# Performance work log

Measured on AMD Instinct MI355X. Metric: run time of the kernel, lower is better.

## Reference

```python
import jax, jax.numpy as jnp
import numpy as np

B = 512
M = 50
N = 50
G = 1            # args.g
ITER = 4         # args.iter_50
EPS = 1e-8


def image2matrix_vit(x):
    # x: [b,1,28,28] -> [b,49,16] (4x4 non-overlapping patches, row-major)
    b = x.shape[0]
    t = x[:, 0].reshape(b, 7, 4, 7, 4)
    return t.transpose(0, 1, 3, 2, 4).reshape(b, 49, 16)


def maxpool2d(x, kh, kw, sh, sw):
    # x: [b,1,H,W], VALID max pooling (matches F.max_pool2d)
    return jax.lax.reduce_window(x, -jnp.inf, jax.lax.max,
                                 (1, 1, kh, kw), (1, 1, sh, sw), 'VALID')


def optical_mvm(inp, w, full_sig):
    # inp: [b,50,50] normalized input, w: [b,50,50] normalized weight (pre-transpose)
    w = jnp.swapaxes(w, 1, 2)
    indim1 = inp.shape[1]       # 50
    odim2 = w.shape[1]          # 50
    out_row = inp.shape[-2]     # 50
    A = jnp.repeat(jnp.repeat(inp, G, axis=1), ITER, axis=2)   # [b,50,200]
    Bm = jnp.repeat(jnp.repeat(w, G, axis=1), ITER, axis=2)    # [b,50,200]
    pr = (4 * M - A.shape[-2]) // 2
    pc = (4 * N - A.shape[-1]) // 2
    A = jnp.pad(A, ((0, 0), (pr, pr), (pc, pc)))               # [b,200,200]
    Bm = jnp.pad(Bm, ((0, 0), (pr, pr), (pc, pc)))
    # precomputed reference spectrum (args.fft_sig_50)
    fft_sig = jnp.fft.fftshift(jnp.fft.fft(full_sig, axis=0), axes=0)
    fft_full = jnp.fft.fftshift(jnp.fft.fft(full_sig[None] * A, axis=1), axes=1)
    opc = fft_full * Bm
    opc_fft = jnp.abs(jnp.fft.fftshift(jnp.fft.fft(opc, axis=2), axes=2))
    r0, r1 = 2 * M - odim2, 2 * M + odim2          # 50:150
    c0, c1 = 2 * N + N // indim1, 3 * N + 3        # 101:153
    temp = opc_fft[:, r0:r1, c0:c1][:, None]       # [b,1,100,52]
    Cmat = maxpool2d(temp, 2, 3, 2, N // indim1)   # [b,1,50,50]
    amp = jnp.abs(fft_sig)[r0:r1, c0:c1][None, None]
    amp = maxpool2d(amp, 2, 3, 2, N // indim1)     # [1,1,50,50]
    amp = amp / (jnp.max(amp) + EPS)
    res = jnp.abs(Cmat / amp)[:, 0]                # [b,50,50]
    res = res / (jnp.max(res, axis=(1, 2), keepdims=True) + EPS)
    return jnp.swapaxes(res, 1, 2)[:, :out_row, :odim2]


def matrix_multiply_optical(inp, w, full_sig):
    # inp: [b,50,50]; w: [50,50] (already abs+padded)
    b = inp.shape[0]
    wb = jnp.broadcast_to(w.T[None], (b,) + w.T.shape)       # [b,50,50]
    imax = jnp.max(inp, axis=-1, keepdims=True)              # [b,50,1]
    inpn = inp / (imax + EPS)
    wmax = jnp.max(wb, axis=-2, keepdims=True)               # [b,1,50]
    wn = wb / (wmax + EPS)
    max_multi = imax @ wmax                                  # [b,50,50]
    out = optical_mvm(inpn, wn, full_sig).astype(jnp.float32)
    return out * max_multi


def setup_inputs() -> dict:
    key = jax.random.key(0)
    k1, k2, k3, k4 = jax.random.split(key, 4)
    inp = jax.random.uniform(k1, (B, 1, 28, 28), dtype=jnp.float32)
    weight = jax.random.normal(k2, (50, 16), dtype=jnp.float32) * 0.1
    bias = jax.random.normal(k3, (1, 49, 50), dtype=jnp.float32) * 0.01
    full_sig = jax.random.uniform(k4, (4 * M, 4 * N), dtype=jnp.float32)
    return {"input": inp, "weight": weight, "bias": bias, "full_sig": full_sig}


def reference(input, weight, bias, full_sig):
    x = image2matrix_vit(input)                  # [b,49,16]
    w = jnp.abs(weight)                          # exp_type != 'standard_mmm'
    out1 = x.shape[1]                            # 49
    x = jnp.pad(x, ((0, 0), (0, 50 - x.shape[1]), (0, 50 - x.shape[2])))
    w = jnp.pad(w, ((0, 50 - w.shape[0]), (0, 50 - w.shape[1])))
    out = matrix_multiply_optical(x, w, full_sig)
    return out[:, :out1, :50] + bias             # bias broadcasts over batch
```

## Files before the change

### kernel.cpp

```cpp
#include <hip/hip_runtime.h>
#include <math.h>

#define EPS 1e-8f
#define TWOPI 6.2831853071795864769f

typedef _Float16 h8 __attribute__((ext_vector_type(8)));
typedef float f32x16 __attribute__((ext_vector_type(16)));

#define WS_WMAX 0
#define WS_WN   64
#define WS_RCPA 1024
#define WS_A2   8192
#define WS_B3   16384


__global__ __launch_bounds__(256) void k_prelude(const float* __restrict__ w,
                                                 const float* __restrict__ fs,
                                                 float* __restrict__ ws) {
    const int blk = blockIdx.x, t = threadIdx.x;
    if (blk < 163) {
        __shared__ float tc[200], tsn[200];
        for (int i = t; i < 200; i += 256) {
            float s, c;
            sincosf(-TWOPI * (float)i / 200.f, &s, &c);
            tc[i] = c; tsn[i] = s;
        }
        __syncthreads();
        int gid = blk * 256 + t;
        int q = gid >> 3, part = gid & 7;
        float aR = 0.f, aI = 0.f;
        if (q < 5200) {
            int s_ = q / 52, u = q - s_ * 52;
            int k = (150 + s_) % 200;
            int j = 101 + u;
            int ph = (k * (part * 25)) % 200;
            for (int r = part * 25; r < part * 25 + 25; ++r) {
                float v = fs[r * 200 + j];
                aR = fmaf(v, tc[ph], aR);
                aI = fmaf(v, tsn[ph], aI);
                ph += k; if (ph >= 200) ph -= 200;
            }
        }
        aR += __shfl_xor(aR, 1); aI += __shfl_xor(aI, 1);
        aR += __shfl_xor(aR, 2); aI += __shfl_xor(aI, 2);
        aR += __shfl_xor(aR, 4); aI += __shfl_xor(aI, 4);
        if (q < 5200 && part == 0)
            ws[WS_RCPA + q] = 1.0f / sqrtf(aR * aR + aI * aI);
    } else {
        int gid = (blk - 163) * 256 + t;
        if (gid < 50) {
            float mx = 0.f, vals[16];
            for (int q = 0; q < 16; ++q) {
                float v = fabsf(w[gid * 16 + q]);
                vals[q] = v; mx = fmaxf(mx, v);
            }
            ws[WS_WMAX + gid] = mx;
            float d = mx + EPS;
            for (int q = 0; q < 16; ++q) ws[WS_WN + gid * 16 + q] = vals[q] / d;
        }
        _Float16* A2h = (_Float16*)(ws + WS_A2);
        for (int a = gid; a < 16384; a += 4096) {
            int s = a & 7, l = (a >> 3) & 63, pks = (a >> 9) & 7, tm = a >> 12;
            int part = pks >> 2;
            int row = 32 * tm + (l & 31);
            int k = 16 * (pks & 3) + 8 * (l >> 5) + s;
            float X = 0.f;
            if (row < 100 && k < 49) {
                int m = (row < 50) ? row : row - 50;
                int kk = (175 + m) % 200;
                int ph = (kk * (75 + k)) % 200;
                float sn, cs;
                sincosf(-TWOPI * (float)ph / 200.f, &sn, &cs);
                X = (row < 50) ? cs : sn;
            }
            _Float16 hi = (_Float16)X;
            A2h[a] = part ? (_Float16)(X - (float)hi) : hi;
        }
        _Float16* B3h = (_Float16*)(ws + WS_B3);
        for (int bI = gid; bI < 32768; bI += 4096) {
            int s = bI & 7, l = (bI >> 3) & 63, pks = (bI >> 9) & 15, tn = bI >> 13;
            int part = pks >> 3;
            int np = 32 * tn + (l & 31);
            int kap = 16 * (pks & 7) + 8 * (l >> 5) + s;
            float X = 0.f;
            if (np < 104) {
                int cc = np >> 1;
                int j = kap & 63;
                int ph = ((cc + 1) * j) % 200;
                float sn, cs;
                sincosf(-TWOPI * (float)ph / 200.f, &sn, &cs);
                X = (np & 1) ? ((kap < 64) ? sn : cs) : ((kap < 64) ? cs : -sn);
            }
            _Float16 hi = (_Float16)X;
            B3h[bI] = part ? (_Float16)(X - (float)hi) : hi;
        }
    }
}

__global__ __launch_bounds__(512, 4) void k_main(const float* __restrict__ in,
                                                 const float* __restrict__ bias,
                                                 const float* __restrict__ fs,
                                                 const float* __restrict__ ws,
                                                 float* __restrict__ out) {
    __shared__ __align__(16) char R1[16384];
    __shared__ __align__(16) char R2[32768];
    __shared__ float xpat[50][16];
    __shared__ float imax_s[50];
    __shared__ float inv_s[50];
    __shared__ float res_s[26][50];
    __shared__ __align__(16) float red8[8];

    const int t = threadIdx.x;
    const int b = blockIdx.x;
    const int lane = t & 63;
    const int wid = t >> 6;
    const int swid = __builtin_amdgcn_readfirstlane(wid);
    const float* ib = in + b * 784;

    if (t < 196) {
        int row = t >> 2, s4 = t & 3;
        int pr = row / 7, pc = row - pr * 7;
        float4 v4 = *(const float4*)(ib + (pr * 4 + s4) * 28 + pc * 4);
        *(float4*)(&xpat[row][s4 * 4]) = v4;
        float mx = fmaxf(fmaxf(v4.x, v4.y), fmaxf(v4.z, v4.w));
        mx = fmaxf(mx, __shfl_xor(mx, 1));
        mx = fmaxf(mx, __shfl_xor(mx, 2));
        if (s4 == 0) { imax_s[row] = mx; inv_s[row] = 1.f / (mx + EPS); }
    }
    __syncthreads();

    {
        const int l = t & 63;
        const int ksq = (t >> 6) & 3;
        const int tn = t >> 8;
        const int j = (l & 31) + 32 * tn;
        const int i0 = 16 * ksq + 8 * (l >> 5);
        h8 hiv, lov;
        #pragma unroll
        for (int s = 0; s < 8; ++s) {
            int i = i0 + s;
            float v = 0.f;
            if (i < 49) v = fs[(75 + i) * 200 + j] * xpat[i][j >> 2] * inv_s[i];
            _Float16 hi = (_Float16)v;
            hiv[s] = hi;
            lov[s] = (_Float16)(v - (float)hi);
        }
        _Float16* B2h = (_Float16*)R1;
        const int base0 = ((tn * 8 + ksq) * 64 + l) * 8;
        *(h8*)(B2h + base0) = hiv;
        *(h8*)(B2h + base0 + 2048) = lov;
    }
    __syncthreads();

    {
        const int tm = swid >> 1, tn = swid & 1;
        f32x16 acc;
        #pragma unroll
        for (int i = 0; i < 16; ++i) acc[i] = 0.f;
        const h8* wsA2 = (const h8*)(ws + WS_A2);
        #pragma unroll
        for (int ks = 0; ks < 12; ++ks) {
            int pA = (ks < 4) ? ks : ks - 4;
            int pB = (ks < 8) ? ks : ks - 8;
            h8 a = wsA2[(tm * 8 + pA) * 64 + lane];
            h8 bf = *(const h8*)(R1 + (((tn * 8 + pB) * 64 + lane) << 4));
            acc = __builtin_amdgcn_mfma_f32_32x32x16_f16(a, bf, acc, 0, 0, 0);
        }
        const float* wn = ws + WS_WN;
        const int j = (lane & 31) + 32 * tn;
        const int q = j >> 2;
        _Float16* A3h = (_Float16*)R2;
        #pragma unroll
        for (int r = 0; r < 16; ++r) {
            int row = (r & 3) + 8 * (r >> 2) + 4 * (lane >> 5) + 32 * tm;
            if (row < 100) {
                int m = (row < 50) ? row : row - 50;
                float v = acc[r] * wn[m * 16 + q];
                _Float16 hi = (_Float16)v;
                int kap = j + ((row < 50) ? 0 : 64);
                int tm3 = m >> 5;
                int pks = kap >> 4;
                int lslot = (m & 31) + 32 * ((kap >> 3) & 1);
                int base = ((tm3 * 16 + pks) * 64 + lslot) * 8 + (kap & 7);
                A3h[base] = hi;
                A3h[base + 4096] = (_Float16)(v - (float)hi);
            }
        }
    }
    __syncthreads();

    {
        const int tm3 = swid >> 2, tn3 = swid & 3;
        f32x16 acc;
        #pragma unroll
        for (int i = 0; i < 16; ++i) acc[i] = 0.f;
        const h8* wsB3 = (const h8*)(ws + WS_B3);
        #pragma unroll
        for (int ks = 0; ks < 24; ++ks) {
            int pA = (ks < 8) ? ks : ks - 8;
            int pB = (ks < 16) ? ks : ks - 16;
            h8 a = *(const h8*)(R2 + (((tm3 * 16 + pA) * 64 + lane) << 4));
            h8 bf = wsB3[(tn3 * 16 + pB) * 64 + lane];
            acc = __builtin_amdgcn_mfma_f32_32x32x16_f16(a, bf, acc, 0, 0, 0);
        }
        const int np = (lane & 31) + 32 * tn3;
        float* aG = (float*)R1;
        if (np < 104) {
            const int cc = np >> 1;
            const bool wr = !(np & 1);
            #pragma unroll
            for (int r = 0; r < 16; ++r) {
                int row = (r & 3) + 8 * (r >> 2) + 4 * (lane >> 5) + 32 * tm3;
                float g = acc[r];
                float gp = __shfl_xor(g, 1);
                if (row < 50 && wr) aG[row * 52 + cc] = sqrtf(g * g + gp * gp);
            }
        }
    }
    __syncthreads();

    const float* ra = ws + WS_RCPA;
    const float* aG = (const float*)R1;
    float local = 0.f;
    for (int o = t; o < 1300; o += 512) {
        int hh = o / 50, w2 = o - hh * 50;
        int h = hh + 12;
        int m1 = 2 * h - 25, m2 = m1 + 1;
        float v = 0.f;
        #pragma unroll
        for (int du = 0; du < 3; ++du) {
            int u = w2 + du;
            if (m1 >= 0) v = fmaxf(v, aG[m1 * 52 + u]);
            if (m2 < 50) v = fmaxf(v, aG[m2 * 52 + u]);
        }
        float rc = ra[(2 * h) * 52 + w2];
        #pragma unroll
        for (int du = 1; du < 3; ++du) rc = fminf(rc, ra[(2 * h) * 52 + w2 + du]);
        #pragma unroll
        for (int du = 0; du < 3; ++du) rc = fminf(rc, ra[(2 * h + 1) * 52 + w2 + du]);
        float r = v * rc;
        res_s[hh][w2] = r;
        local = fmaxf(local, r);
    }
    #pragma unroll
    for (int off = 32; off > 0; off >>= 1)
        local = fmaxf(local, __shfl_xor(local, off));
    if (lane == 0) red8[wid] = local;
    __syncthreads();

    float mres;
    {
        float4 r0 = *(const float4*)&red8[0];
        float4 r1 = *(const float4*)&red8[4];
        float m0 = fmaxf(fmaxf(r0.x, r0.y), fmaxf(r0.z, r0.w));
        float m1 = fmaxf(fmaxf(r1.x, r1.y), fmaxf(r1.z, r1.w));
        mres = fmaxf(m0, m1);
    }
    float invm = 1.f / (mres + EPS);

    const float* wmaxg = ws + WS_WMAX;
    for (int o = t; o < 2450; o += 512) {
        int r = o / 50, c = o - r * 50;
        float val = bias[o];
        if (c >= 12 && c < 38)
            val = fmaf(res_s[c - 12][r] * invm, imax_s[r] * wmaxg[c], val);
        out[b * 2450 + o] = val;
    }
}

extern "C" void kernel_launch(void* const* d_in, const int* in_sizes, int n_in,
                              void* d_out, int out_size, void* d_ws, size_t ws_size,
                              hipStream_t stream) {
    const float* in   = (const float*)d_in[0];
    const float* w    = (const float*)d_in[1];
    const float* bias = (const float*)d_in[2];
    const float* fs   = (const float*)d_in[3];
    float* out = (float*)d_out;
    float* ws  = (float*)d_ws;

    hipLaunchKernelGGL(k_prelude, dim3(179),  dim3(256), 0, stream, w, fs, ws);
    hipLaunchKernelGGL(k_main,    dim3(512),  dim3(512), 0, stream, in, bias, fs, ws, out);
}
```

Measured before the change: 25.99 us.

## Drop split-fp16 on one operand of each GEMM and pad LDS layout

Both MFMA GEMM stages previously used hi+lo fp16 splitting on both operands (three MFMA products per step). Now one operand per GEMM is stored as plain fp16 and only the other keeps its hi/lo split, which cuts the MFMA count from 12 to 8 and from 24 to 16. The work is spread over two independent accumulators. The A3 LDS tile shrinks to half size with a padded stride of 65 to avoid bank conflicts, and it is zero-initialized up front. The prelude grid grows so each thread writes a single A2 element. The trade-off is reduced precision on the DFT-twiddle or intermediate operand.

```diff
diff --git a/kernel.cpp b/kernel.cpp
--- a/kernel.cpp
+++ b/kernel.cpp
@@ -58,12 +58,12 @@
             float d = mx + EPS;
             for (int q = 0; q < 16; ++q) ws[WS_WN + gid * 16 + q] = vals[q] / d;
         }
-        _Float16* A2h = (_Float16*)(ws + WS_A2);
-        for (int a = gid; a < 16384; a += 4096) {
-            int s = a & 7, l = (a >> 3) & 63, pks = (a >> 9) & 7, tm = a >> 12;
-            int part = pks >> 2;
+        {
+            _Float16* A2h = (_Float16*)(ws + WS_A2);
+            int a = gid;
+            int s = a & 7, l = (a >> 3) & 63, pks = (a >> 9) & 3, tm = a >> 11;
             int row = 32 * tm + (l & 31);
-            int k = 16 * (pks & 3) + 8 * (l >> 5) + s;
+            int k = 16 * pks + 8 * (l >> 5) + s;
             float X = 0.f;
             if (row < 100 && k < 49) {
                 int m = (row < 50) ? row : row - 50;
@@ -73,11 +73,10 @@
                 sincosf(-TWOPI * (float)ph / 200.f, &sn, &cs);
                 X = (row < 50) ? cs : sn;
             }
-            _Float16 hi = (_Float16)X;
-            A2h[a] = part ? (_Float16)(X - (float)hi) : hi;
+            A2h[a] = (_Float16)X;
         }
         _Float16* B3h = (_Float16*)(ws + WS_B3);
-        for (int bI = gid; bI < 32768; bI += 4096) {
+        for (int bI = gid; bI < 32768; bI += 8192) {
             int s = bI & 7, l = (bI >> 3) & 63, pks = (bI >> 9) & 15, tn = bI >> 13;
             int part = pks >> 3;
             int np = 32 * tn + (l & 31);
@@ -103,7 +102,7 @@
                                                  const float* __restrict__ ws,
                                                  float* __restrict__ out) {
     __shared__ __align__(16) char R1[16384];
-    __shared__ __align__(16) char R2[32768];
+    __shared__ __align__(16) char R2[16640];
     __shared__ float xpat[50][16];
     __shared__ float imax_s[50];
     __shared__ float inv_s[50];
@@ -127,6 +126,12 @@
         mx = fmaxf(mx, __shfl_xor(mx, 2));
         if (s4 == 0) { imax_s[row] = mx; inv_s[row] = 1.f / (mx + EPS); }
     }
+    {
+        h8 z;
+        #pragma unroll
+        for (int s = 0; s < 8; ++s) z[s] = (_Float16)0.f;
+        for (int o = t; o < 1040; o += 512) *(h8*)(R2 + (o << 4)) = z;
+    }
     __syncthreads();
 
     {
@@ -154,18 +159,19 @@
 
     {
         const int tm = swid >> 1, tn = swid & 1;
-        f32x16 acc;
-        #pragma unroll
-        for (int i = 0; i < 16; ++i) acc[i] = 0.f;
+        f32x16 acc0, acc1;
+        #pragma unroll
+        for (int i = 0; i < 16; ++i) { acc0[i] = 0.f; acc1[i] = 0.f; }
         const h8* wsA2 = (const h8*)(ws + WS_A2);
         #pragma unroll
-        for (int ks = 0; ks < 12; ++ks) {
-            int pA = (ks < 4) ? ks : ks - 4;
-            int pB = (ks < 8) ? ks : ks - 8;
-            h8 a = wsA2[(tm * 8 + pA) * 64 + lane];
-            h8 bf = *(const h8*)(R1 + (((tn * 8 + pB) * 64 + lane) << 4));
-            acc = __builtin_amdgcn_mfma_f32_32x32x16_f16(a, bf, acc, 0, 0, 0);
-        }
+        for (int kq = 0; kq < 4; ++kq) {
+            h8 a   = wsA2[(tm * 4 + kq) * 64 + lane];
+            h8 bhi = *(const h8*)(R1 + (((tn * 8 + kq) * 64 + lane) << 4));
+            h8 blo = *(const h8*)(R1 + (((tn * 8 + kq + 4) * 64 + lane) << 4));
+            acc0 = __builtin_amdgcn_mfma_f32_32x32x16_f16(a, bhi, acc0, 0, 0, 0);
+            acc1 = __builtin_amdgcn_mfma_f32_32x32x16_f16(a, blo, acc1, 0, 0, 0);
+        }
+        f32x16 acc = acc0 + acc1;
         const float* wn = ws + WS_WN;
         const int j = (lane & 31) + 32 * tn;
         const int q = j >> 2;
@@ -176,14 +182,12 @@
             if (row < 100) {
                 int m = (row < 50) ? row : row - 50;
                 float v = acc[r] * wn[m * 16 + q];
-                _Float16 hi = (_Float16)v;
                 int kap = j + ((row < 50) ? 0 : 64);
                 int tm3 = m >> 5;
                 int pks = kap >> 4;
-                int lslot = (m & 31) + 32 * ((kap >> 3) & 1);
-                int base = ((tm3 * 16 + pks) * 64 + lslot) * 8 + (kap & 7);
-                A3h[base] = hi;
-                A3h[base + 4096] = (_Float16)(v - (float)hi);
+                int bb = (kap >> 3) & 1;
+                int elem = ((tm3 * 8 + pks) * 65 + (m & 31) + 33 * bb) * 8 + (kap & 7);
+                A3h[elem] = (_Float16)v;
             }
         }
     }
@@ -191,18 +195,20 @@
 
     {
         const int tm3 = swid >> 2, tn3 = swid & 3;
-        f32x16 acc;
-        #pragma unroll
-        for (int i = 0; i < 16; ++i) acc[i] = 0.f;
+        f32x16 acc0, acc1;
+        #pragma unroll
+        for (int i = 0; i < 16; ++i) { acc0[i] = 0.f; acc1[i] = 0.f; }
         const h8* wsB3 = (const h8*)(ws + WS_B3);
-        #pragma unroll
-        for (int ks = 0; ks < 24; ++ks) {
-            int pA = (ks < 8) ? ks : ks - 8;
-            int pB = (ks < 16) ? ks : ks - 16;
-            h8 a = *(const h8*)(R2 + (((tm3 * 16 + pA) * 64 + lane) << 4));
-            h8 bf = wsB3[(tn3 * 16 + pB) * 64 + lane];
-            acc = __builtin_amdgcn_mfma_f32_32x32x16_f16(a, bf, acc, 0, 0, 0);
-        }
+        const int aoff = lane + (lane >> 5);
+        #pragma unroll
+        for (int kq = 0; kq < 8; ++kq) {
+            h8 a   = *(const h8*)(R2 + (((tm3 * 8 + kq) * 65 + aoff) << 4));
+            h8 bhi = wsB3[(tn3 * 16 + kq) * 64 + lane];
+            h8 blo = wsB3[(tn3 * 16 + kq + 8) * 64 + lane];
+            acc0 = __builtin_amdgcn_mfma_f32_32x32x16_f16(a, bhi, acc0, 0, 0, 0);
+            acc1 = __builtin_amdgcn_mfma_f32_32x32x16_f16(a, blo, acc1, 0, 0, 0);
+        }
+        f32x16 acc = acc0 + acc1;
         const int np = (lane & 31) + 32 * tn3;
         float* aG = (float*)R1;
         if (np < 104) {
@@ -278,6 +284,6 @@
     float* out = (float*)d_out;
     float* ws  = (float*)d_ws;
 
-    hipLaunchKernelGGL(k_prelude, dim3(179),  dim3(256), 0, stream, w, fs, ws);
+    hipLaunchKernelGGL(k_prelude, dim3(195),  dim3(256), 0, stream, w, fs, ws);
     hipLaunchKernelGGL(k_main,    dim3(512),  dim3(512), 0, stream, in, bias, fs, ws, out);
 }
```

Result: faster. 24.81 us (-4.5%).
